# Optimization experiments

Hardware: AMD Instinct MI355X
Metric: run time of the kernel (lower is better)

## Reference

```python
import jax, jax.numpy as jnp
import numpy as np

EMB = 512
HEADS = 8
QKV = 512
WIN = 256  # 'range' init arg, >1 so W = range


def setup_inputs() -> dict:
    key = jax.random.key(0)
    ks = jax.random.split(key, 9)
    B, N = 2, 4096
    s_in = 1.0 / np.sqrt(EMB)
    s_qkv = 1.0 / np.sqrt(QKV)
    return {
        "x": jax.random.normal(ks[0], (B, N, EMB), jnp.float32),
        "Wq": jax.random.normal(ks[1], (EMB, QKV), jnp.float32) * s_in,
        "bq": jnp.zeros((QKV,), jnp.float32),
        "Wk": jax.random.normal(ks[2], (EMB, QKV), jnp.float32) * s_in,
        "bk": jnp.zeros((QKV,), jnp.float32),
        "Wv": jax.random.normal(ks[3], (EMB, QKV), jnp.float32) * s_in,
        "bv": jnp.zeros((QKV,), jnp.float32),
        "Wfc": jax.random.normal(ks[4], (QKV, EMB), jnp.float32) * s_qkv,
        "bfc": jnp.zeros((EMB,), jnp.float32),
    }


def reference(x, Wq, bq, Wk, bk, Wv, bv, Wfc, bfc):
    B, N, E = x.shape
    hd = QKV // HEADS  # head dim = 64
    # window mask: |i-j| <= W//2 -> 0 else -inf
    idx = jnp.arange(N)
    inwin = jnp.abs(idx[None, :] - idx[:, None]) <= (WIN // 2)
    M = jnp.where(inwin, 0.0, -jnp.inf).astype(x.dtype)  # [N,N]

    def split(h):  # [B,N,QKV] -> [B,H,N,hd]
        return h.reshape(B, N, HEADS, hd).transpose(0, 2, 1, 3)

    q = split(x @ Wq + bq)
    k = split(x @ Wk + bk)
    v = split(x @ Wv + bv)

    scale = 1.0 / np.sqrt(hd)
    attn = jnp.einsum("bhnd,bhmd->bhnm", q, k) * scale + M
    attn = jax.nn.softmax(attn, axis=-1)
    o = jnp.einsum("bhnm,bhmd->bhnd", attn, v)  # [B,H,N,hd]
    o = o.transpose(0, 2, 1, 3).reshape(B, N, QKV)
    return o @ Wfc + bfc
```

## Files before the change

kernel.cpp:

```cpp
#include <hip/hip_runtime.h>
#include <math.h>

typedef __bf16 bf16;
typedef __attribute__((ext_vector_type(8))) __bf16 bf16x8;
typedef __attribute__((ext_vector_type(4))) float f32x4;

#define N_SEQ 4096
#define NEGINF -1e30f

__device__ __forceinline__ void gl_lds16(const void* g, void* l) {
    __builtin_amdgcn_global_load_lds(
        (const __attribute__((address_space(1))) void*)g,
        (__attribute__((address_space(3))) void*)l, 16, 0, 0);
}

__device__ __forceinline__ bf16x8 frag64(const bf16* base, int row, int g) {
    return *(const bf16x8*)(base + (row << 6) + ((g ^ (row & 7)) << 3));
}

__global__ __launch_bounds__(256) void prep_k(
    const float* __restrict__ x, bf16* __restrict__ xb,
    const float* __restrict__ Wq, const float* __restrict__ bq,
    const float* __restrict__ Wk, const float* __restrict__ bk,
    const float* __restrict__ Wv, const float* __restrict__ bv,
    const float* __restrict__ Wfc, const float* __restrict__ bfc,
    bf16* __restrict__ Wcat, float* __restrict__ bcat) {
    __shared__ bf16 tile[64][65];
    const int t = threadIdx.x;
    const int bx = blockIdx.x;
    if (bx < 2048) {
        int idx = bx * 256 + t;
        const float4* xv = (const float4*)x;
        float4 a = xv[idx * 2], b = xv[idx * 2 + 1];
        bf16x8 o;
        o[0] = (bf16)a.x; o[1] = (bf16)a.y; o[2] = (bf16)a.z; o[3] = (bf16)a.w;
        o[4] = (bf16)b.x; o[5] = (bf16)b.y; o[6] = (bf16)b.z; o[7] = (bf16)b.w;
        ((bf16x8*)xb)[idx] = o;
        return;
    }
    const int bz = bx - 2048;
    const int k0 = (bz & 7) << 6, n0 = (bz >> 3) << 6;
    const int sel = n0 >> 9, nloc = n0 & 511;
    const float* W = (sel == 0) ? Wq : (sel == 1) ? Wk : (sel == 2) ? Wv : Wfc;
    const float* bi = (sel == 0) ? bq : (sel == 1) ? bk : (sel == 2) ? bv : bfc;
#pragma unroll
    for (int i = 0; i < 16; i++) {
        int idx = (i << 8) + t;
        int r = idx >> 6, c = idx & 63;
        tile[r][c] = (bf16)W[(size_t)(k0 + r) * 512 + nloc + c];
    }
    __syncthreads();
#pragma unroll
    for (int i = 0; i < 16; i++) {
        int idx = (i << 8) + t;
        int r = idx >> 6, c = idx & 63;
        Wcat[(size_t)(n0 + r) * 512 + k0 + c] = tile[c][r];
    }
    if ((bz & 7) == 0 && t < 64) bcat[n0 + t] = bi[nloc + t];
}

template <int OUT, int BN, int NT>
__global__ __launch_bounds__(256, 3) void gemm_bf16_k(
    const bf16* __restrict__ A, const bf16* __restrict__ Bt,
    const float* __restrict__ bias, void* __restrict__ Cout) {
    constexpr int NI = BN / 32;
    __shared__ __align__(16) bf16 smem[16384];
    bf16* sA = smem;
    bf16* sB = smem + 8192;
    const int t = threadIdx.x;
    const int lane = t & 63, wid = t >> 6;
    const int wr = wid >> 1, wc = wid & 1;
    const int wg = blockIdx.x;
    const int s = (wg & 7) * (8 * NT) + (wg >> 3);
    const int m_idx = s / NT, n_idx = s - m_idx * NT;
    const int m0 = m_idx << 7, n0 = n_idx * BN;

    f32x4 acc[4][NI] = {};

    const bf16* Ag = A + ((size_t)m0 << 9);
    const bf16* Bg = Bt + ((size_t)n0 << 9);

    for (int kt = 0; kt < 8; kt++) {
        const int k0 = kt << 6;
#pragma unroll
        for (int i = 0; i < 4; i++) {
            int gid = (i << 8) + t;
            int row = gid >> 3, gs = ((gid & 7) ^ (row & 7)) << 3;
            gl_lds16(Ag + ((size_t)row << 9) + k0 + gs, &sA[gid << 3]);
        }
#pragma unroll
        for (int i = 0; i < NI; i++) {
            int gid = (i << 8) + t;
            int row = gid >> 3, gs = ((gid & 7) ^ (row & 7)) << 3;
            gl_lds16(Bg + ((size_t)row << 9) + k0 + gs, &sB[gid << 3]);
        }
        __syncthreads();
#pragma unroll
        for (int ks = 0; ks < 2; ks++) {
            int g = (ks << 2) + (lane >> 4);
            bf16x8 af[4], bfr[NI];
#pragma unroll
            for (int mi = 0; mi < 4; mi++)
                af[mi] = frag64(sA, (wr << 6) + (mi << 4) + (lane & 15), g);
#pragma unroll
            for (int ni = 0; ni < NI; ni++)
                bfr[ni] = frag64(sB, wc * (BN / 2) + (ni << 4) + (lane & 15), g);
#pragma unroll
            for (int mi = 0; mi < 4; mi++)
#pragma unroll
                for (int ni = 0; ni < NI; ni++)
                    acc[mi][ni] = __builtin_amdgcn_mfma_f32_16x16x32_bf16(
                        af[mi], bfr[ni], acc[mi][ni], 0, 0, 0);
        }
        __syncthreads();
    }

    float bb[NI];
#pragma unroll
    for (int ni = 0; ni < NI; ni++)
        bb[ni] = bias[n0 + wc * (BN / 2) + (ni << 4) + (lane & 15)];

    if (OUT == 0) {
        bf16* cs = smem;
#pragma unroll
        for (int mi = 0; mi < 4; mi++)
#pragma unroll
            for (int ni = 0; ni < NI; ni++)
#pragma unroll
                for (int r = 0; r < 4; r++) {
                    int row = (wr << 6) + (mi << 4) + ((lane >> 4) << 2) + r;
                    int col = (wc << 6) + (ni << 4) + (lane & 15);
                    int g = col >> 3;
                    cs[(row << 7) + ((g ^ (row & 7)) << 3) + (col & 7)] =
                        (bf16)(acc[mi][ni][r] + bb[ni]);
                }
        __syncthreads();
        int row = t >> 1, half = t & 1;
        int gm = m0 + row;
        int b = gm >> 12, n = gm & 4095;
#pragma unroll
        for (int j = 0; j < 8; j++) {
            int g = (half << 3) + j;
            bf16x8 v = *(bf16x8*)&cs[(row << 7) + ((g ^ (row & 7)) << 3)];
            int gc = n0 + (g << 3);
            int sel = gc >> 9, rem = gc & 511;
            int h = rem >> 6, d = rem & 63;
            *(bf16x8*)&(
                ((bf16*)Cout)[(((size_t)((sel << 4) + (b << 3) + h) * 4096 + n)
                               << 6) +
                              d]) = v;
        }
    } else {
        float* cs = (float*)smem;
#pragma unroll
        for (int mi = 0; mi < 4; mi++)
#pragma unroll
            for (int ni = 0; ni < NI; ni++)
#pragma unroll
                for (int r = 0; r < 4; r++) {
                    int row = (wr << 6) + (mi << 4) + ((lane >> 4) << 2) + r;
                    int col = (wc << 5) + (ni << 4) + (lane & 15);
                    int g4 = col >> 2;
                    cs[(row << 6) + ((g4 ^ (row & 7)) << 2) + (col & 3)] =
                        acc[mi][ni][r] + bb[ni];
                }
        __syncthreads();
        int row = t >> 1, half = t & 1;
#pragma unroll
        for (int j = 0; j < 8; j++) {
            int g4 = (half << 3) + j;
            f32x4 v = *(f32x4*)&cs[(row << 6) + ((g4 ^ (row & 7)) << 2)];
            *(f32x4*)&(
                ((float*)Cout)[(size_t)(m0 + row) * 512 + n0 + (g4 << 2)]) = v;
        }
    }
}

__global__ __launch_bounds__(256) void attn_bf16_k(
    const bf16* __restrict__ Q, const bf16* __restrict__ K,
    const bf16* __restrict__ V, bf16* __restrict__ O) {
    __shared__ bf16 QP[8192];
    __shared__ bf16 Ks[2][4096];
    __shared__ bf16 VT[2][4096];

    const int t = threadIdx.x;
    const int lane = t & 63, wid = t >> 6;
    const int wg = blockIdx.x;
    const int sblk = ((wg & 7) << 6) + (wg >> 3);
    const int bh = sblk >> 5;
    const int q0 = (sblk & 31) << 7;

    const bf16* Qp = Q + ((size_t)bh << 18);
    const bf16* Kp = K + ((size_t)bh << 18);
    const bf16* Vp = V + ((size_t)bh << 18);

#pragma unroll
    for (int i = 0; i < 4; i++) {
        int gid = (i << 8) + t;
        int row = gid >> 3, gs = ((gid & 7) ^ (row & 7)) << 3;
        gl_lds16(Qp + ((size_t)(q0 + row) << 6) + gs, &QP[gid << 3]);
    }
    __syncthreads();

    bf16x8 aq[2][2];
#pragma unroll
    for (int b = 0; b < 2; b++)
#pragma unroll
        for (int ks = 0; ks < 2; ks++)
            aq[b][ks] = frag64(QP, (wid << 5) + (b << 4) + (lane & 15),
                               (ks << 2) + (lane >> 4));

    float mrun[2][4], lrun[2][4];
    f32x4 acc_o[2][4] = {};
#pragma unroll
    for (int b = 0; b < 2; b++)
#pragma unroll
        for (int r = 0; r < 4; r++) { mrun[b][r] = NEGINF; lrun[b][r] = 0.f; }

    const int cstart = (q0 >= 128) ? q0 - 128 : 0;
    const int cend = (q0 + 256 <= N_SEQ) ? q0 + 256 : N_SEQ;
    const int nch = (cend - cstart) >> 6;

#define STAGE_KV(c0, sb)                                                     \
    {                                                                        \
        _Pragma("unroll") for (int i = 0; i < 2; i++) {                      \
            int gid = (i << 8) + t;                                          \
            int row = gid >> 3, gs = ((gid & 7) ^ (row & 7)) << 3;           \
            gl_lds16(Kp + ((size_t)((c0) + row) << 6) + gs,                  \
                     &Ks[sb][gid << 3]);                                     \
        }                                                                    \
        int key = t >> 2;                                                    \
        int gd0 = (t & 3) << 1;                                              \
        const uint4* vs = (const uint4*)(Vp + ((size_t)((c0) + key) << 6));  \
        union { uint4 u; bf16 h[8]; } u0, u1;                                \
        u0.u = vs[gd0]; u1.u = vs[gd0 + 1];                                  \
        _Pragma("unroll") for (int e = 0; e < 8; e++) {                      \
            int d0 = (gd0 << 3) + e;                                         \
            VT[sb][(d0 << 6) + (((key >> 3) ^ (d0 & 7)) << 3) + (key & 7)] = \
                u0.h[e];                                                     \
            int d1 = d0 + 8;                                                 \
            VT[sb][(d1 << 6) + (((key >> 3) ^ (d1 & 7)) << 3) + (key & 7)] = \
                u1.h[e];                                                     \
        }                                                                    \
    }

    STAGE_KV(cstart, 0);

    int buf = 0;
    for (int tch = 0; tch < nch; tch++) {
        const int c0 = cstart + (tch << 6);
        __syncthreads();
        if (tch + 1 < nch) STAGE_KV(c0 + 64, buf ^ 1);

        const int rel = c0 - q0;
        const bool masked = (rel != 0) && (rel != 64);

#pragma unroll
        for (int b = 0; b < 2; b++) {
            f32x4 s[4] = {};
#pragma unroll
            for (int ks = 0; ks < 2; ks++) {
                int g = (ks << 2) + (lane >> 4);
#pragma unroll
                for (int ni = 0; ni < 4; ni++) {
                    bf16x8 bk = frag64(&Ks[buf][0], (ni << 4) + (lane & 15), g);
                    s[ni] = __builtin_amdgcn_mfma_f32_16x16x32_bf16(
                        aq[b][ks], bk, s[ni], 0, 0, 0);
                }
            }

            bf16* Pw = &QP[((wid << 1) + b) << 10];
#pragma unroll
            for (int r = 0; r < 4; r++) {
                int rowl = ((lane >> 4) << 2) + r;
                int qi = q0 + (wid << 5) + (b << 4) + rowl;
                float v[4];
                if (masked) {
#pragma unroll
                    for (int ni = 0; ni < 4; ni++) {
                        int kj = c0 + (ni << 4) + (lane & 15);
                        int dd = qi - kj;
                        v[ni] = (dd <= 128 && dd >= -128) ? s[ni][r] * 0.125f
                                                          : NEGINF;
                    }
                } else {
#pragma unroll
                    for (int ni = 0; ni < 4; ni++) v[ni] = s[ni][r] * 0.125f;
                }
                float mx = fmaxf(fmaxf(v[0], v[1]), fmaxf(v[2], v[3]));
#pragma unroll
                for (int off = 1; off < 16; off <<= 1)
                    mx = fmaxf(mx, __shfl_xor(mx, off));
                float mn = fmaxf(mrun[b][r], mx);
                float alpha = __expf(mrun[b][r] - mn);
                float rs = 0.f;
#pragma unroll
                for (int ni = 0; ni < 4; ni++) {
                    float p = __expf(v[ni] - mn);
                    rs += p;
                    int col = (ni << 4) + (lane & 15);
                    Pw[(rowl << 6) + (((col >> 3) ^ (rowl & 7)) << 3) +
                       (col & 7)] = (bf16)p;
                }
#pragma unroll
                for (int off = 1; off < 16; off <<= 1)
                    rs += __shfl_xor(rs, off);
                mrun[b][r] = mn;
                lrun[b][r] = lrun[b][r] * alpha + rs;
#pragma unroll
                for (int nd = 0; nd < 4; nd++) acc_o[b][nd][r] *= alpha;
            }

#pragma unroll
            for (int ks = 0; ks < 2; ks++) {
                int g = (ks << 2) + (lane >> 4);
                bf16x8 pa = frag64(Pw, lane & 15, g);
#pragma unroll
                for (int nd = 0; nd < 4; nd++) {
                    bf16x8 bv = frag64(&VT[buf][0], (nd << 4) + (lane & 15), g);
                    acc_o[b][nd] = __builtin_amdgcn_mfma_f32_16x16x32_bf16(
                        pa, bv, acc_o[b][nd], 0, 0, 0);
                }
            }
        }
        buf ^= 1;
    }
#undef STAGE_KV

    const int bb = bh >> 3, h = bh & 7;
#pragma unroll
    for (int b = 0; b < 2; b++) {
#pragma unroll
        for (int r = 0; r < 4; r++) {
            float inv = 1.f / lrun[b][r];
            int n = q0 + (wid << 5) + (b << 4) + ((lane >> 4) << 2) + r;
#pragma unroll
            for (int nd = 0; nd < 4; nd++) {
                int d = (nd << 4) + (lane & 15);
                O[(((size_t)(bb * 4096 + n)) << 9) + (h << 6) + d] =
                    (bf16)(acc_o[b][nd][r] * inv);
            }
        }
    }
}

extern "C" void kernel_launch(void* const* d_in, const int* in_sizes, int n_in,
                              void* d_out, int out_size, void* d_ws, size_t ws_size,
                              hipStream_t stream) {
    (void)in_sizes; (void)n_in; (void)out_size; (void)ws_size;
    const float* x   = (const float*)d_in[0];
    const float* Wq  = (const float*)d_in[1];
    const float* bq  = (const float*)d_in[2];
    const float* Wk  = (const float*)d_in[3];
    const float* bk  = (const float*)d_in[4];
    const float* Wv  = (const float*)d_in[5];
    const float* bv  = (const float*)d_in[6];
    const float* Wfc = (const float*)d_in[7];
    const float* bfc = (const float*)d_in[8];

    bf16* xb    = (bf16*)d_ws;
    bf16* Wcat  = xb + (size_t)8192 * 512;
    float* bcat = (float*)(Wcat + (size_t)2048 * 512);
    bf16* QKVb  = (bf16*)(bcat + 2048);
    bf16* Ob    = QKVb + (size_t)3 * 16 * 4096 * 64;

    prep_k<<<2304, 256, 0, stream>>>(x, xb, Wq, bq, Wk, bk, Wv, bv, Wfc, bfc,
                                     Wcat, bcat);

    gemm_bf16_k<0, 128, 12><<<768, 256, 0, stream>>>(xb, Wcat, bcat, QKVb);

    const bf16* Qb = QKVb;
    const bf16* Kb = QKVb + ((size_t)1 << 22);
    const bf16* Vb = QKVb + ((size_t)2 << 22);
    attn_bf16_k<<<512, 256, 0, stream>>>(Qb, Kb, Vb, Ob);

    gemm_bf16_k<1, 64, 8><<<512, 256, 0, stream>>>(
        Ob, Wcat + ((size_t)1536 << 9), bcat + 1536, d_out);
}
```

Measured before the change: 153.7 us.

## Write V transposed from QKV GEMM epilogue and async-load it in attention

The QKV projection GEMM now writes the V third of its output in a transposed [bh][d][n] layout through a transposed LDS staging step. The attention kernel can then stage V^T tiles with direct global-to-LDS 16-byte loads instead of loading V rows and scattering elements into LDS one by one. This removes per-element LDS transpose stores from the attention inner loop. The cost is moved into the GEMM epilogue, which now does a scattered transposed LDS write for the V blocks.

```diff
diff --git a/kernel.cpp b/kernel.cpp
--- a/kernel.cpp
+++ b/kernel.cpp
@@ -62,7 +62,8 @@
 template <int OUT, int BN, int NT>
 __global__ __launch_bounds__(256, 3) void gemm_bf16_k(
     const bf16* __restrict__ A, const bf16* __restrict__ Bt,
-    const float* __restrict__ bias, void* __restrict__ Cout) {
+    const float* __restrict__ bias, void* __restrict__ Cout,
+    bf16* __restrict__ VTg) {
     constexpr int NI = BN / 32;
     __shared__ __align__(16) bf16 smem[16384];
     bf16* sA = smem;
@@ -121,34 +122,63 @@
         bb[ni] = bias[n0 + wc * (BN / 2) + (ni << 4) + (lane & 15)];
 
     if (OUT == 0) {
-        bf16* cs = smem;
-#pragma unroll
-        for (int mi = 0; mi < 4; mi++)
-#pragma unroll
-            for (int ni = 0; ni < NI; ni++)
-#pragma unroll
-                for (int r = 0; r < 4; r++) {
-                    int row = (wr << 6) + (mi << 4) + ((lane >> 4) << 2) + r;
-                    int col = (wc << 6) + (ni << 4) + (lane & 15);
-                    int g = col >> 3;
-                    cs[(row << 7) + ((g ^ (row & 7)) << 3) + (col & 7)] =
-                        (bf16)(acc[mi][ni][r] + bb[ni]);
-                }
-        __syncthreads();
-        int row = t >> 1, half = t & 1;
-        int gm = m0 + row;
-        int b = gm >> 12, n = gm & 4095;
-#pragma unroll
-        for (int j = 0; j < 8; j++) {
-            int g = (half << 3) + j;
-            bf16x8 v = *(bf16x8*)&cs[(row << 7) + ((g ^ (row & 7)) << 3)];
-            int gc = n0 + (g << 3);
-            int sel = gc >> 9, rem = gc & 511;
+        if (n0 < 1024) {
+            bf16* cs = smem;
+#pragma unroll
+            for (int mi = 0; mi < 4; mi++)
+#pragma unroll
+                for (int ni = 0; ni < NI; ni++)
+#pragma unroll
+                    for (int r = 0; r < 4; r++) {
+                        int row = (wr << 6) + (mi << 4) + ((lane >> 4) << 2) + r;
+                        int col = (wc << 6) + (ni << 4) + (lane & 15);
+                        int g = col >> 3;
+                        cs[(row << 7) + ((g ^ (row & 7)) << 3) + (col & 7)] =
+                            (bf16)(acc[mi][ni][r] + bb[ni]);
+                    }
+            __syncthreads();
+            int row = t >> 1, half = t & 1;
+            int gm = m0 + row;
+            int b = gm >> 12, n = gm & 4095;
+#pragma unroll
+            for (int j = 0; j < 8; j++) {
+                int g = (half << 3) + j;
+                bf16x8 v = *(bf16x8*)&cs[(row << 7) + ((g ^ (row & 7)) << 3)];
+                int gc = n0 + (g << 3);
+                int sel = gc >> 9, rem = gc & 511;
+                int h = rem >> 6, d = rem & 63;
+                *(bf16x8*)&(((bf16*)Cout)[(((size_t)((sel << 4) + (b << 3) + h) *
+                                                4096 +
+                                            n)
+                                           << 6) +
+                                          d]) = v;
+            }
+        } else {
+            bf16* cs = smem;
+#pragma unroll
+            for (int mi = 0; mi < 4; mi++)
+#pragma unroll
+                for (int ni = 0; ni < NI; ni++)
+#pragma unroll
+                    for (int r = 0; r < 4; r++) {
+                        int row = (wr << 6) + (mi << 4) + ((lane >> 4) << 2) + r;
+                        int col = (wc << 6) + (ni << 4) + (lane & 15);
+                        cs[(col << 7) + (((row >> 3) ^ (col & 7)) << 3) +
+                           (row & 7)] = (bf16)(acc[mi][ni][r] + bb[ni]);
+                    }
+            __syncthreads();
+            int dp = t >> 1, half = t & 1;
+            int rem = (n0 - 1024) + dp;
             int h = rem >> 6, d = rem & 63;
-            *(bf16x8*)&(
-                ((bf16*)Cout)[(((size_t)((sel << 4) + (b << 3) + h) * 4096 + n)
-                               << 6) +
-                              d]) = v;
+            int b = m0 >> 12;
+            size_t rowbase =
+                ((size_t)(((b << 3) + h) << 6) + d) * 4096 + (m0 & 4095);
+#pragma unroll
+            for (int j = 0; j < 8; j++) {
+                int g = (half << 3) + j;
+                bf16x8 v = *(bf16x8*)&cs[(dp << 7) + ((g ^ (dp & 7)) << 3)];
+                *(bf16x8*)&VTg[rowbase + (g << 3)] = v;
+            }
         }
     } else {
         float* cs = (float*)smem;
@@ -178,7 +208,7 @@
 
 __global__ __launch_bounds__(256) void attn_bf16_k(
     const bf16* __restrict__ Q, const bf16* __restrict__ K,
-    const bf16* __restrict__ V, bf16* __restrict__ O) {
+    const bf16* __restrict__ VTglob, bf16* __restrict__ O) {
     __shared__ bf16 QP[8192];
     __shared__ bf16 Ks[2][4096];
     __shared__ bf16 VT[2][4096];
@@ -192,7 +222,7 @@
 
     const bf16* Qp = Q + ((size_t)bh << 18);
     const bf16* Kp = K + ((size_t)bh << 18);
-    const bf16* Vp = V + ((size_t)bh << 18);
+    const bf16* VTp = VTglob + ((size_t)bh << 18);
 
 #pragma unroll
     for (int i = 0; i < 4; i++) {
@@ -229,18 +259,11 @@
             gl_lds16(Kp + ((size_t)((c0) + row) << 6) + gs,                  \
                      &Ks[sb][gid << 3]);                                     \
         }                                                                    \
-        int key = t >> 2;                                                    \
-        int gd0 = (t & 3) << 1;                                              \
-        const uint4* vs = (const uint4*)(Vp + ((size_t)((c0) + key) << 6));  \
-        union { uint4 u; bf16 h[8]; } u0, u1;                                \
-        u0.u = vs[gd0]; u1.u = vs[gd0 + 1];                                  \
-        _Pragma("unroll") for (int e = 0; e < 8; e++) {                      \
-            int d0 = (gd0 << 3) + e;                                         \
-            VT[sb][(d0 << 6) + (((key >> 3) ^ (d0 & 7)) << 3) + (key & 7)] = \
-                u0.h[e];                                                     \
-            int d1 = d0 + 8;                                                 \
-            VT[sb][(d1 << 6) + (((key >> 3) ^ (d1 & 7)) << 3) + (key & 7)] = \
-                u1.h[e];                                                     \
+        _Pragma("unroll") for (int i = 0; i < 2; i++) {                      \
+            int gid = (i << 8) + t;                                          \
+            int row = gid >> 3, gs = ((gid & 7) ^ (row & 7)) << 3;           \
+            gl_lds16(VTp + (size_t)row * 4096 + (c0) + gs,                   \
+                     &VT[sb][gid << 3]);                                     \
         }                                                                    \
     }
 
@@ -362,18 +385,18 @@
     bf16* Wcat  = xb + (size_t)8192 * 512;
     float* bcat = (float*)(Wcat + (size_t)2048 * 512);
     bf16* QKVb  = (bf16*)(bcat + 2048);
-    bf16* Ob    = QKVb + (size_t)3 * 16 * 4096 * 64;
+    bf16* VTg   = QKVb + ((size_t)2 << 22);
+    bf16* Ob    = QKVb + ((size_t)3 << 22);
 
     prep_k<<<2304, 256, 0, stream>>>(x, xb, Wq, bq, Wk, bk, Wv, bv, Wfc, bfc,
                                      Wcat, bcat);
 
-    gemm_bf16_k<0, 128, 12><<<768, 256, 0, stream>>>(xb, Wcat, bcat, QKVb);
+    gemm_bf16_k<0, 128, 12><<<768, 256, 0, stream>>>(xb, Wcat, bcat, QKVb, VTg);
 
     const bf16* Qb = QKVb;
     const bf16* Kb = QKVb + ((size_t)1 << 22);
-    const bf16* Vb = QKVb + ((size_t)2 << 22);
-    attn_bf16_k<<<512, 256, 0, stream>>>(Qb, Kb, Vb, Ob);
+    attn_bf16_k<<<512, 256, 0, stream>>>(Qb, Kb, VTg, Ob);
 
     gemm_bf16_k<1, 64, 8><<<512, 256, 0, stream>>>(
-        Ob, Wcat + ((size_t)1536 << 9), bcat + 1536, d_out);
-}
+        Ob, Wcat + ((size_t)1536 << 9), bcat + 1536, d_out, nullptr);
+}
```

After: 153.7 us. Within noise of the previous version (+0.0%).
